# Optimization experiments

Measured on AMD Instinct MI355X. Metric: run time of the kernel, lower is better.

## Reference

```python
import jax, jax.numpy as jnp
import numpy as np

H = 128          # hidden_size
B = 64           # batch of users
T = 20           # current-session length (== max_sess_len)
S = 10           # friend sessions per user (graph degree)
L = 20           # max_sess_len
NUM_ITEMS = 50000
NUM_USERS = 10000
TOPK = 2         # topk in sess_similarity


def gru(x, W_ih, W_hh, b_ih, b_hh):
    """torch nn.GRU (1 layer, batch_first). x: [N, T, H] -> outputs [N, T, H], h_T [N, H]."""
    h0 = jnp.zeros((x.shape[0], x.shape[-1]), x.dtype)

    def step(h, xt):
        gi = xt @ W_ih.T + b_ih          # [N, 3H]
        gh = h @ W_hh.T + b_hh
        i_r, i_z, i_n = jnp.split(gi, 3, axis=-1)
        h_r, h_z, h_n = jnp.split(gh, 3, axis=-1)
        r = jax.nn.sigmoid(i_r + h_r)
        z = jax.nn.sigmoid(i_z + h_z)
        n = jnp.tanh(i_n + r * h_n)
        h = (1.0 - z) * n + z * h
        return h, h

    hT, ys = jax.lax.scan(step, h0, jnp.swapaxes(x, 0, 1))
    return jnp.swapaxes(ys, 0, 1), hT


def masked_softmax(x, mask, axis):
    neg = jnp.finfo(x.dtype).min
    return jax.nn.softmax(jnp.where(mask, x, neg), axis=axis)


def setup_inputs() -> dict:
    key = jax.random.key(0)
    ks = jax.random.split(key, 12)
    users = jax.random.randint(ks[0], (B,), 0, NUM_USERS)
    cur_sess = jax.random.randint(ks[1], (B, T), 0, NUM_ITEMS)          # all valid -> full length
    hist_sess = jax.random.randint(ks[2], (B, S, L), 0, NUM_ITEMS)
    frds_sess = jax.random.randint(ks[3], (B, S, L), 0, NUM_ITEMS)
    cur_sess_len = jnp.full((B,), T, dtype=jnp.int32)
    # parameters
    v_emb = jax.random.uniform(ks[4], (NUM_ITEMS + 1, H), minval=-1.0, maxval=1.0)
    v_emb = v_emb.at[NUM_ITEMS].set(0.0)                                 # padding_idx row
    u_emb = jax.random.normal(ks[5], (NUM_USERS, H)) * (1.0 / np.sqrt(H))
    sc = 1.0 / np.sqrt(H)
    W_ih = jax.random.normal(ks[6], (3 * H, H)) * sc
    W_hh = jax.random.normal(ks[7], (3 * H, H)) * sc
    b_ih = jnp.zeros((3 * H,), jnp.float32)
    b_hh = jnp.zeros((3 * H,), jnp.float32)
    out1_w = jax.random.normal(ks[8], (NUM_ITEMS, 3 * H)) * (1.0 / np.sqrt(3 * H))
    out1_b = jnp.zeros((NUM_ITEMS,), jnp.float32)
    return dict(users=users, cur_sess=cur_sess, hist_sess=hist_sess, frds_sess=frds_sess,
                cur_sess_len=cur_sess_len, v_emb=v_emb, u_emb=u_emb,
                W_ih=W_ih, W_hh=W_hh, b_ih=b_ih, b_hh=b_hh, out1_w=out1_w, out1_b=out1_b)


def reference(users, cur_sess, hist_sess, frds_sess, cur_sess_len,
              v_emb, u_emb, W_ih, W_hh, b_ih, b_hh, out1_w, out1_b):
    # --- rnn_encoder on current session (dropout p=0, eval) ---
    hs, _ = gru(v_emb[cur_sess], W_ih, W_hh, b_ih, b_hh)                 # [B, T, H]
    query = hs

    # --- friend branch (hist branch is dead: hu is overwritten with zeros) ---
    # sess_encoder: GRU over each friend session's items
    frd_items = v_emb[frds_sess]                                         # [B, S, L, H]
    enc, _ = gru(frd_items.reshape(B * S, L, H), W_ih, W_hh, b_ih, b_hh)
    enc = enc.reshape(B, S, L, H)                                        # encoder_output

    # sess_similarity: max over session positions, softmax over degree (S)
    scores = jnp.einsum('bth,bslh->bstl', query, enc)                    # [B, S, T, L]
    sim_raw = scores.max(axis=-1)                                        # [B, S, T]
    sim1 = jax.nn.softmax(sim_raw, axis=1)
    # preserve: edges that are top-2 most similar for ANY step t (S > TOPK branch)
    _, idx = jax.lax.top_k(jnp.swapaxes(sim1, 1, 2), TOPK)               # [B, T, 2]
    preserve = jax.nn.one_hot(idx, S, dtype=jnp.float32).sum((1, 2)) > 0 # [B, S]

    # sess_embedding_attn on the filtered subgraph (masking == filtering here)
    user_e = u_emb[users]                                                # [B, H]
    w = jax.nn.softmax(jnp.einsum('bh,bslh->bsl', user_e, frd_items), axis=2)
    sess_emb = jnp.einsum('bsl,bslh->bsh', w, frd_items)                 # [B, S, H]

    # user_sess_reduce_func: sim1 (pre-filter softmax values), then two softmaxes
    # over the surviving edges (masked softmax over S)
    m = preserve[:, :, None]                                             # [B, S, 1]
    s = masked_softmax(sim1, m, axis=1)
    s = masked_softmax(s, m, axis=1)
    s = jnp.where(m, s, 0.0)
    hf = jnp.einsum('bst,bsh->bth', s, sess_emb)                         # [B, T, H]

    hu = jnp.zeros_like(hs)                                              # hu = zeros_like(hs)
    output = jnp.concatenate([hs, hu, hf], axis=-1)                      # [B, T, 3H]
    logits = output @ out1_w.T + out1_b                                  # [B, T, NUM_ITEMS]
    return logits
```

## Files before the change

kernel.cpp:

```cpp
#include <hip/hip_runtime.h>
#include <cstdint>
#include <cstddef>

#define H_      128
#define B_      64
#define T_      20
#define S_      10
#define L_      20
#define NITEMS  50000
#define NSEQ    704
#define NTOK    (NSEQ * 20)
#define NPAD    50048
#define KA      256

typedef __attribute__((ext_vector_type(8))) short short8;
typedef __attribute__((ext_vector_type(4))) float f32x4;

__device__ __forceinline__ unsigned short f2bf(float f) {
  unsigned int u = __float_as_uint(f);
  u += 0x7FFF + ((u >> 16) & 1);
  return (unsigned short)(u >> 16);
}
__device__ __forceinline__ float sigmoidf_(float x) {
  return 1.0f / (1.0f + __expf(-x));
}

__global__ void __launch_bounds__(256) k1_convert_w(const float* __restrict__ w,
                                                    unsigned short* __restrict__ wb) {
  int t = blockIdx.x * 256 + threadIdx.x;
  int n = t >> 5, kc = t & 31;
  int k0 = kc * 8;
  unsigned int o0, o1, o2, o3;
  if (n < NITEMS) {
    int src = (k0 < 128) ? k0 : (k0 + 128);
    const float* p = w + (size_t)n * 384 + src;
    float4 f0 = *(const float4*)p;
    float4 f1 = *(const float4*)(p + 4);
    o0 = (unsigned)f2bf(f0.x) | ((unsigned)f2bf(f0.y) << 16);
    o1 = (unsigned)f2bf(f0.z) | ((unsigned)f2bf(f0.w) << 16);
    o2 = (unsigned)f2bf(f1.x) | ((unsigned)f2bf(f1.y) << 16);
    o3 = (unsigned)f2bf(f1.z) | ((unsigned)f2bf(f1.w) << 16);
  } else {
    o0 = o1 = o2 = o3 = 0u;
  }
  *(uint4*)(wb + (size_t)n * 256 + k0) = make_uint4(o0, o1, o2, o3);
}

__global__ void __launch_bounds__(384) k2_gi(const int* __restrict__ cur,
                                             const int* __restrict__ frd,
                                             const float* __restrict__ vemb,
                                             const float* __restrict__ Wih,
                                             const float* __restrict__ bih,
                                             float* __restrict__ gi) {
  __shared__ float xs[16 * 128];
  __shared__ int ids[16];
  int tid = threadIdx.x;
  int tok0 = blockIdx.x * 16;
  if (tid < 16) {
    int tok = tok0 + tid;
    int seq = tok / 20, tt = tok % 20;
    ids[tid] = (seq < 64) ? cur[seq * 20 + tt] : frd[(seq - 64) * 20 + tt];
  }
  __syncthreads();
  for (int idx = tid; idx < 512; idx += 384) {
    int i = idx >> 5, kc = idx & 31;
    *(float4*)&xs[i * 128 + kc * 4] =
        *(const float4*)&vemb[(size_t)ids[i] * 128 + kc * 4];
  }
  __syncthreads();
  int j = tid;
  float acc[16];
#pragma unroll
  for (int i = 0; i < 16; i++) acc[i] = 0.f;
  const float* wrow = Wih + (size_t)j * 128;
  for (int kc = 0; kc < 32; kc++) {
    float4 w4 = *(const float4*)(wrow + kc * 4);
#pragma unroll
    for (int i = 0; i < 16; i++) {
      float4 x4 = *(const float4*)&xs[i * 128 + kc * 4];
      acc[i] += w4.x * x4.x + w4.y * x4.y + w4.z * x4.z + w4.w * x4.w;
    }
  }
  float bb = bih[j];
#pragma unroll
  for (int i = 0; i < 16; i++)
    gi[(size_t)(tok0 + i) * 384 + j] = acc[i] + bb;
}

__global__ void __launch_bounds__(384) k3_gru(const float* __restrict__ Whh,
                                              const float* __restrict__ bhh,
                                              const float* __restrict__ gi,
                                              float* __restrict__ out_h) {
  __shared__ float hb[3 * 128];
  __shared__ float pre[3 * 256];
  __shared__ float gin[3 * 128];
  __shared__ float ghn[3 * 128];
  int j = threadIdx.x;
  int seq0 = blockIdx.x * 3;
  int G = NSEQ - seq0; if (G > 3) G = 3;
  float4 wv[32];
  const float4* wr = (const float4*)(Whh + (size_t)j * 128);
#pragma unroll
  for (int kc = 0; kc < 32; kc++) wv[kc] = wr[kc];
  float bb = bhh[j];
  if (j < 128) { hb[j] = 0.f; hb[128 + j] = 0.f; hb[256 + j] = 0.f; }
  __syncthreads();
  for (int t = 0; t < 20; t++) {
    for (int g = 0; g < G; g++) {
      float acc = bb;
#pragma unroll
      for (int kc = 0; kc < 32; kc++) {
        float4 h4 = *(const float4*)&hb[g * 128 + kc * 4];
        float4 w4 = wv[kc];
        acc += w4.x * h4.x + w4.y * h4.y + w4.z * h4.z + w4.w * h4.w;
      }
      float gv = gi[(size_t)((seq0 + g) * 20 + t) * 384 + j];
      if (j < 256) pre[g * 256 + j] = gv + acc;
      else { gin[g * 128 + (j - 256)] = gv; ghn[g * 128 + (j - 256)] = acc; }
    }
    __syncthreads();
    if (j < 128) {
      for (int g = 0; g < G; g++) {
        float r = sigmoidf_(pre[g * 256 + j]);
        float z = sigmoidf_(pre[g * 256 + 128 + j]);
        float n = tanhf(gin[g * 128 + j] + r * ghn[g * 128 + j]);
        float hN = (1.f - z) * n + z * hb[g * 128 + j];
        hb[g * 128 + j] = hN;
        out_h[(size_t)((seq0 + g) * 20 + t) * 128 + j] = hN;
      }
    }
    __syncthreads();
  }
}

__global__ void __launch_bounds__(256) k4_scores(const float* __restrict__ out_h,
                                                 float* __restrict__ sim_raw) {
  __shared__ float qs[20 * 132];
  __shared__ float es[20 * 132];
  __shared__ float sc[400];
  int tid = threadIdx.x;
  int b = blockIdx.x / 10, s = blockIdx.x % 10;
  int eseq = 64 + b * 10 + s;
  for (int idx = tid; idx < 640; idx += 256) {
    int row = idx >> 5, kc = idx & 31;
    *(float4*)&qs[row * 132 + kc * 4] =
        *(const float4*)&out_h[(size_t)(b * 20 + row) * 128 + kc * 4];
    *(float4*)&es[row * 132 + kc * 4] =
        *(const float4*)&out_h[(size_t)(eseq * 20 + row) * 128 + kc * 4];
  }
  __syncthreads();
  for (int idx = tid; idx < 400; idx += 256) {
    int t = idx / 20, l = idx % 20;
    float acc = 0.f;
#pragma unroll
    for (int kc = 0; kc < 32; kc++) {
      float4 q4 = *(const float4*)&qs[t * 132 + kc * 4];
      float4 e4 = *(const float4*)&es[l * 132 + kc * 4];
      acc += q4.x * e4.x + q4.y * e4.y + q4.z * e4.z + q4.w * e4.w;
    }
    sc[idx] = acc;
  }
  __syncthreads();
  if (tid < 20) {
    float m = sc[tid * 20];
    for (int l = 1; l < 20; l++) m = fmaxf(m, sc[tid * 20 + l]);
    sim_raw[(size_t)(b * 10 + s) * 20 + tid] = m;
  }
}

__global__ void __launch_bounds__(64) k5_soft(const float* __restrict__ sim_raw,
                                              float* __restrict__ sfin) {
  __shared__ float sv[200];
  __shared__ float s1[200];
  __shared__ int pres[10];
  int tid = threadIdx.x;
  int b = blockIdx.x;
  for (int idx = tid; idx < 200; idx += 64) sv[idx] = sim_raw[(size_t)b * 200 + idx];
  if (tid < 10) pres[tid] = 0;
  __syncthreads();
  if (tid < 20) {
    int t = tid;
    float mx = -3.4e38f;
    for (int s = 0; s < 10; s++) mx = fmaxf(mx, sv[s * 20 + t]);
    float sum = 0.f;
    for (int s = 0; s < 10; s++) sum += __expf(sv[s * 20 + t] - mx);
    float inv = 1.0f / sum;
    float v1 = -1.f, v2 = -1.f; int i1 = 0, i2 = 0;
    for (int s = 0; s < 10; s++) {
      float v = __expf(sv[s * 20 + t] - mx) * inv;
      s1[s * 20 + t] = v;
      if (v > v1) { v2 = v1; i2 = i1; v1 = v; i1 = s; }
      else if (v > v2) { v2 = v; i2 = s; }
    }
    atomicOr(&pres[i1], 1);
    atomicOr(&pres[i2], 1);
  }
  __syncthreads();
  if (tid < 20) {
    int t = tid;
    float mx = -3.4e38f;
    for (int s = 0; s < 10; s++) if (pres[s]) mx = fmaxf(mx, s1[s * 20 + t]);
    float sum = 0.f;
    for (int s = 0; s < 10; s++) if (pres[s]) sum += __expf(s1[s * 20 + t] - mx);
    float inv = 1.f / sum;
    float mx2 = -3.4e38f;
    for (int s = 0; s < 10; s++)
      if (pres[s]) mx2 = fmaxf(mx2, __expf(s1[s * 20 + t] - mx) * inv);
    float sum2 = 0.f;
    for (int s = 0; s < 10; s++)
      if (pres[s]) sum2 += __expf(__expf(s1[s * 20 + t] - mx) * inv - mx2);
    float inv2 = 1.f / sum2;
    for (int s = 0; s < 10; s++) {
      float o = 0.f;
      if (pres[s]) o = __expf(__expf(s1[s * 20 + t] - mx) * inv - mx2) * inv2;
      sfin[(size_t)(b * 10 + s) * 20 + t] = o;
    }
  }
}

__global__ void __launch_bounds__(128) k6_sess(const int* __restrict__ users,
                                               const int* __restrict__ frd,
                                               const float* __restrict__ vemb,
                                               const float* __restrict__ uemb,
                                               float* __restrict__ sess) {
  __shared__ float fs[20 * 132];
  __shared__ float us[128];
  __shared__ float dt[20];
  __shared__ float wl[20];
  __shared__ int fid[20];
  int tid = threadIdx.x;
  int b = blockIdx.x / 10, s = blockIdx.x % 10;
  if (tid < 20) fid[tid] = frd[(size_t)(b * 10 + s) * 20 + tid];
  us[tid] = uemb[(size_t)users[b] * 128 + tid];
  __syncthreads();
  for (int idx = tid; idx < 640; idx += 128) {
    int row = idx >> 5, kc = idx & 31;
    *(float4*)&fs[row * 132 + kc * 4] =
        *(const float4*)&vemb[(size_t)fid[row] * 128 + kc * 4];
  }
  __syncthreads();
  if (tid < 20) {
    float acc = 0.f;
    for (int kc = 0; kc < 32; kc++) {
      float4 u4 = *(const float4*)&us[kc * 4];
      float4 f4 = *(const float4*)&fs[tid * 132 + kc * 4];
      acc += u4.x * f4.x + u4.y * f4.y + u4.z * f4.z + u4.w * f4.w;
    }
    dt[tid] = acc;
  }
  __syncthreads();
  if (tid < 20) {
    float mx = -3.4e38f;
    for (int l = 0; l < 20; l++) mx = fmaxf(mx, dt[l]);
    float sum = 0.f;
    for (int l = 0; l < 20; l++) sum += __expf(dt[l] - mx);
    wl[tid] = __expf(dt[tid] - mx) / sum;
  }
  __syncthreads();
  float acc = 0.f;
  for (int l = 0; l < 20; l++) acc += wl[l] * fs[l * 132 + tid];
  sess[(size_t)(b * 10 + s) * 128 + tid] = acc;
}

__global__ void __launch_bounds__(256) k7_hf(const float* __restrict__ sfin,
                                             const float* __restrict__ sess,
                                             float* __restrict__ hf) {
  __shared__ float sf[200];
  __shared__ float se[10 * 128];
  int tid = threadIdx.x;
  int b = blockIdx.x;
  for (int idx = tid; idx < 200; idx += 256) sf[idx] = sfin[(size_t)b * 200 + idx];
  for (int idx = tid; idx < 1280; idx += 256) se[idx] = sess[(size_t)b * 1280 + idx];
  __syncthreads();
  for (int idx = tid; idx < 2560; idx += 256) {
    int t = idx >> 7, h = idx & 127;
    float acc = 0.f;
#pragma unroll
    for (int s = 0; s < 10; s++) acc += sf[s * 20 + t] * se[s * 128 + h];
    hf[(size_t)b * 2560 + idx] = acc;
  }
}

__global__ void __launch_bounds__(256) k8_act(const float* __restrict__ out_h,
                                              const float* __restrict__ hf,
                                              unsigned int* __restrict__ act) {
  int g = blockIdx.x * 256 + threadIdx.x;
  int m = g >> 7, p = g & 127;
  float a0, a1;
  if (p < 64) {
    a0 = out_h[(size_t)m * 128 + p * 2];
    a1 = out_h[(size_t)m * 128 + p * 2 + 1];
  } else {
    a0 = hf[(size_t)m * 128 + (p - 64) * 2];
    a1 = hf[(size_t)m * 128 + (p - 64) * 2 + 1];
  }
  act[g] = (unsigned)f2bf(a0) | ((unsigned)f2bf(a1) << 16);
}

__device__ __forceinline__ void async_cp16(const unsigned short* g, unsigned short* l) {
  __builtin_amdgcn_global_load_lds((__attribute__((address_space(1))) void*)g,
                                   (__attribute__((address_space(3))) void*)l,
                                   16, 0, 0);
}

__global__ void __launch_bounds__(256) k9_gemm(const unsigned short* __restrict__ act,
                                               const unsigned short* __restrict__ wb,
                                               const float* __restrict__ bias,
                                               float* __restrict__ out) {
  __shared__ __align__(16) unsigned short Bs[128 * 256];
  __shared__ __align__(16) unsigned short As[128 * 40];
  int tid = threadIdx.x;
  int w = tid >> 6, lane = tid & 63;
  int q = (lane >> 4) & 3, c = lane & 15;
  int wm = w >> 1, wn = w & 1;
  int nb0 = blockIdx.x * 128;

#pragma unroll
  for (int i = 0; i < 16; i++) {
    int n_l = i * 8 + w * 2 + (lane >> 5);
    int p = lane & 31;
    int kc = p ^ (n_l & 31);
    async_cp16(wb + (size_t)(nb0 + n_l) * 256 + kc * 8,
               &Bs[(i * 8 + w * 2) * 256]);
  }

  float bs[4]; int okn[4]; int ncol[4];
#pragma unroll
  for (int nt = 0; nt < 4; nt++) {
    int n = nb0 + wn * 64 + nt * 16 + c;
    ncol[nt] = n;
    okn[nt] = (n < NITEMS);
    bs[nt] = (n < NITEMS) ? bias[n] : 0.f;
  }

  for (int mc = 0; mc < 10; mc++) {
    f32x4 acc[4][4];
#pragma unroll
    for (int mt = 0; mt < 4; mt++)
#pragma unroll
      for (int nt = 0; nt < 4; nt++) {
        f32x4 z = {0.f, 0.f, 0.f, 0.f};
        acc[mt][nt] = z;
      }
    for (int kf = 0; kf < 8; kf++) {
      __syncthreads();
      {
        int ch0 = tid * 2;
#pragma unroll
        for (int jj = 0; jj < 2; jj++) {
          int ch = ch0 + jj;
          int row = ch >> 2, kk = ch & 3;
          short8 v = *(const short8*)&act[(size_t)(mc * 128 + row) * 256 + kf * 32 + kk * 8];
          *(short8*)&As[row * 40 + kk * 8] = v;
        }
      }
      __syncthreads();
      short8 bfr[4];
#pragma unroll
      for (int nt = 0; nt < 4; nt++) {
        int n_l = wn * 64 + nt * 16 + c;
        int slot = n_l * 32 + ((kf * 4 + q) ^ (n_l & 31));
        bfr[nt] = *(const short8*)&Bs[slot * 8];
      }
#pragma unroll
      for (int mt = 0; mt < 4; mt++) {
        int row = wm * 64 + mt * 16 + c;
        short8 af = *(const short8*)&As[row * 40 + q * 8];
#pragma unroll
        for (int nt = 0; nt < 4; nt++)
          acc[mt][nt] = __builtin_amdgcn_mfma_f32_16x16x32_bf16(af, bfr[nt], acc[mt][nt], 0, 0, 0);
      }
    }
#pragma unroll
    for (int nt = 0; nt < 4; nt++) {
      if (okn[nt]) {
#pragma unroll
        for (int mt = 0; mt < 4; mt++) {
          int m = mc * 128 + wm * 64 + mt * 16 + q * 4;
#pragma unroll
          for (int r = 0; r < 4; r++)
            out[(size_t)(m + r) * NITEMS + ncol[nt]] = acc[mt][nt][r] + bs[nt];
        }
      }
    }
  }
}

extern "C" void kernel_launch(void* const* d_in, const int* in_sizes, int n_in,
                              void* d_out, int out_size, void* d_ws, size_t ws_size,
                              hipStream_t stream) {
  const int*   users = (const int*)d_in[0];
  const int*   cur   = (const int*)d_in[1];
  const int*   frd   = (const int*)d_in[3];
  const float* vemb  = (const float*)d_in[5];
  const float* uemb  = (const float*)d_in[6];
  const float* Wih   = (const float*)d_in[7];
  const float* Whh   = (const float*)d_in[8];
  const float* bih   = (const float*)d_in[9];
  const float* bhh   = (const float*)d_in[10];
  const float* w1    = (const float*)d_in[11];
  const float* b1    = (const float*)d_in[12];
  float* out = (float*)d_out;

  char* ws = (char*)d_ws;
  size_t off = 0;
  auto alloc = [&](size_t bytes) -> void* {
    void* p = ws + off;
    off = (off + bytes + 255) & ~(size_t)255;
    return p;
  };
  unsigned short* wb   = (unsigned short*)alloc((size_t)NPAD * 256 * 2);
  unsigned int*   act  = (unsigned int*)alloc((size_t)1280 * 128 * 4);
  float*          gi   = (float*)alloc((size_t)NTOK * 384 * 4);
  float*          outh = (float*)alloc((size_t)NTOK * 128 * 4);
  float*          simr = (float*)alloc((size_t)12800 * 4);
  float*          sfin = (float*)alloc((size_t)12800 * 4);
  float*          sess = (float*)alloc((size_t)640 * 128 * 4);
  float*          hf   = (float*)alloc((size_t)1280 * 128 * 4);

  k1_convert_w<<<NPAD / 8, 256, 0, stream>>>(w1, wb);
  k2_gi<<<NTOK / 16, 384, 0, stream>>>(cur, frd, vemb, Wih, bih, gi);
  k3_gru<<<(NSEQ + 2) / 3, 384, 0, stream>>>(Whh, bhh, gi, outh);
  k4_scores<<<640, 256, 0, stream>>>(outh, simr);
  k5_soft<<<64, 64, 0, stream>>>(simr, sfin);
  k6_sess<<<640, 128, 0, stream>>>(users, frd, vemb, uemb, sess);
  k7_hf<<<64, 256, 0, stream>>>(sfin, sess, hf);
  k8_act<<<640, 256, 0, stream>>>(outh, hf, act);
  k9_gemm<<<NPAD / 128, 256, 0, stream>>>((const unsigned short*)act, wb, b1, out);
}
```

Baseline: 522.7 us.

## Fuse fp32-to-bf16 weight conversion into GEMM tile load, retile input-gate kernel

Removes the separate weight-conversion kernel and its bf16 workspace. The GEMM now reads the fp32 output weights directly, converts them to bf16 in registers and writes them into the swizzled LDS tile, replacing the async global-to-LDS copies. This drops one full write and re-read of the converted weight matrix, at the cost of synchronous loads inside the GEMM prologue. The input-gate kernel is also retiled so each thread computes two weight rows over half the tokens, which raises reuse of each shared-memory activation load.

```diff
diff --git a/kernel.cpp b/kernel.cpp
--- a/kernel.cpp
+++ b/kernel.cpp
@@ -25,27 +25,6 @@
   return 1.0f / (1.0f + __expf(-x));
 }
 
-__global__ void __launch_bounds__(256) k1_convert_w(const float* __restrict__ w,
-                                                    unsigned short* __restrict__ wb) {
-  int t = blockIdx.x * 256 + threadIdx.x;
-  int n = t >> 5, kc = t & 31;
-  int k0 = kc * 8;
-  unsigned int o0, o1, o2, o3;
-  if (n < NITEMS) {
-    int src = (k0 < 128) ? k0 : (k0 + 128);
-    const float* p = w + (size_t)n * 384 + src;
-    float4 f0 = *(const float4*)p;
-    float4 f1 = *(const float4*)(p + 4);
-    o0 = (unsigned)f2bf(f0.x) | ((unsigned)f2bf(f0.y) << 16);
-    o1 = (unsigned)f2bf(f0.z) | ((unsigned)f2bf(f0.w) << 16);
-    o2 = (unsigned)f2bf(f1.x) | ((unsigned)f2bf(f1.y) << 16);
-    o3 = (unsigned)f2bf(f1.z) | ((unsigned)f2bf(f1.w) << 16);
-  } else {
-    o0 = o1 = o2 = o3 = 0u;
-  }
-  *(uint4*)(wb + (size_t)n * 256 + k0) = make_uint4(o0, o1, o2, o3);
-}
-
 __global__ void __launch_bounds__(384) k2_gi(const int* __restrict__ cur,
                                              const int* __restrict__ frd,
                                              const float* __restrict__ vemb,
@@ -68,23 +47,31 @@
         *(const float4*)&vemb[(size_t)ids[i] * 128 + kc * 4];
   }
   __syncthreads();
-  int j = tid;
-  float acc[16];
-#pragma unroll
-  for (int i = 0; i < 16; i++) acc[i] = 0.f;
-  const float* wrow = Wih + (size_t)j * 128;
+  int j  = tid % 192;
+  int th = tid / 192;
+  float acc0[8], acc1[8];
+#pragma unroll
+  for (int i = 0; i < 8; i++) { acc0[i] = 0.f; acc1[i] = 0.f; }
+  const float* wr0 = Wih + (size_t)j * 128;
+  const float* wr1 = Wih + (size_t)(j + 192) * 128;
+  const float* xb = &xs[th * 8 * 128];
   for (int kc = 0; kc < 32; kc++) {
-    float4 w4 = *(const float4*)(wrow + kc * 4);
-#pragma unroll
-    for (int i = 0; i < 16; i++) {
-      float4 x4 = *(const float4*)&xs[i * 128 + kc * 4];
-      acc[i] += w4.x * x4.x + w4.y * x4.y + w4.z * x4.z + w4.w * x4.w;
-    }
-  }
-  float bb = bih[j];
-#pragma unroll
-  for (int i = 0; i < 16; i++)
-    gi[(size_t)(tok0 + i) * 384 + j] = acc[i] + bb;
+    float4 wa = *(const float4*)(wr0 + kc * 4);
+    float4 wc = *(const float4*)(wr1 + kc * 4);
+#pragma unroll
+    for (int i = 0; i < 8; i++) {
+      float4 x4 = *(const float4*)&xb[i * 128 + kc * 4];
+      acc0[i] += wa.x * x4.x + wa.y * x4.y + wa.z * x4.z + wa.w * x4.w;
+      acc1[i] += wc.x * x4.x + wc.y * x4.y + wc.z * x4.z + wc.w * x4.w;
+    }
+  }
+  float ba = bih[j], bc = bih[j + 192];
+#pragma unroll
+  for (int i = 0; i < 8; i++) {
+    size_t row = (size_t)(tok0 + th * 8 + i) * 384;
+    gi[row + j]       = acc0[i] + ba;
+    gi[row + j + 192] = acc1[i] + bc;
+  }
 }
 
 __global__ void __launch_bounds__(384) k3_gru(const float* __restrict__ Whh,
@@ -297,14 +284,8 @@
   act[g] = (unsigned)f2bf(a0) | ((unsigned)f2bf(a1) << 16);
 }
 
-__device__ __forceinline__ void async_cp16(const unsigned short* g, unsigned short* l) {
-  __builtin_amdgcn_global_load_lds((__attribute__((address_space(1))) void*)g,
-                                   (__attribute__((address_space(3))) void*)l,
-                                   16, 0, 0);
-}
-
 __global__ void __launch_bounds__(256) k9_gemm(const unsigned short* __restrict__ act,
-                                               const unsigned short* __restrict__ wb,
+                                               const float* __restrict__ w1,
                                                const float* __restrict__ bias,
                                                float* __restrict__ out) {
   __shared__ __align__(16) unsigned short Bs[128 * 256];
@@ -315,13 +296,28 @@
   int wm = w >> 1, wn = w & 1;
   int nb0 = blockIdx.x * 128;
 
-#pragma unroll
-  for (int i = 0; i < 16; i++) {
-    int n_l = i * 8 + w * 2 + (lane >> 5);
-    int p = lane & 31;
-    int kc = p ^ (n_l & 31);
-    async_cp16(wb + (size_t)(nb0 + n_l) * 256 + kc * 8,
-               &Bs[(i * 8 + w * 2) * 256]);
+  {
+    int kc = tid & 31;
+    int src = (kc < 16) ? kc * 8 : kc * 8 + 128;
+#pragma unroll 4
+    for (int i = 0; i < 16; i++) {
+      int row = i * 8 + (tid >> 5);
+      int n = nb0 + row;
+      unsigned int o0, o1, o2, o3;
+      if (n < NITEMS) {
+        const float* p = w1 + (size_t)n * 384 + src;
+        float4 f0 = *(const float4*)p;
+        float4 f1 = *(const float4*)(p + 4);
+        o0 = (unsigned)f2bf(f0.x) | ((unsigned)f2bf(f0.y) << 16);
+        o1 = (unsigned)f2bf(f0.z) | ((unsigned)f2bf(f0.w) << 16);
+        o2 = (unsigned)f2bf(f1.x) | ((unsigned)f2bf(f1.y) << 16);
+        o3 = (unsigned)f2bf(f1.z) | ((unsigned)f2bf(f1.w) << 16);
+      } else {
+        o0 = o1 = o2 = o3 = 0u;
+      }
+      int slot = kc ^ (row & 31);
+      *(uint4*)&Bs[row * 256 + slot * 8] = make_uint4(o0, o1, o2, o3);
+    }
   }
 
   float bs[4]; int okn[4]; int ncol[4];
@@ -409,7 +405,6 @@
     off = (off + bytes + 255) & ~(size_t)255;
     return p;
   };
-  unsigned short* wb   = (unsigned short*)alloc((size_t)NPAD * 256 * 2);
   unsigned int*   act  = (unsigned int*)alloc((size_t)1280 * 128 * 4);
   float*          gi   = (float*)alloc((size_t)NTOK * 384 * 4);
   float*          outh = (float*)alloc((size_t)NTOK * 128 * 4);
@@ -418,7 +413,6 @@
   float*          sess = (float*)alloc((size_t)640 * 128 * 4);
   float*          hf   = (float*)alloc((size_t)1280 * 128 * 4);
 
-  k1_convert_w<<<NPAD / 8, 256, 0, stream>>>(w1, wb);
   k2_gi<<<NTOK / 16, 384, 0, stream>>>(cur, frd, vemb, Wih, bih, gi);
   k3_gru<<<(NSEQ + 2) / 3, 384, 0, stream>>>(Whh, bhh, gi, outh);
   k4_scores<<<640, 256, 0, stream>>>(outh, simr);
@@ -426,5 +420,5 @@
   k6_sess<<<640, 128, 0, stream>>>(users, frd, vemb, uemb, sess);
   k7_hf<<<64, 256, 0, stream>>>(sfin, sess, hf);
   k8_act<<<640, 256, 0, stream>>>(outh, hf, act);
-  k9_gemm<<<NPAD / 128, 256, 0, stream>>>((const unsigned short*)act, wb, b1, out);
-}
+  k9_gemm<<<NPAD / 128, 256, 0, stream>>>((const unsigned short*)act, w1, b1, out);
+}
```

New measurement: 530.8 us. Within noise of the previous version (+1.6%).
